# Kernel optimization log

Hardware: AMD Instinct MI355X
Metric: run time of the kernel (lower is better)

The kernel has to match this reference:

```python
import jax, jax.numpy as jnp
import numpy as np

NUM_EXPERTS = 8
TOP_K = 2
D_MODEL = 1024
D_FF = 4096
TOKENS = 8192


def setup_inputs() -> dict:
    key = jax.random.key(0)
    ks = jax.random.split(key, 7)
    s_in = 1.0 / np.sqrt(D_MODEL)
    s_ff = 1.0 / np.sqrt(D_FF)
    return {
        "x": jax.random.normal(ks[0], (TOKENS, D_MODEL), dtype=jnp.float32),
        "gate_w": jax.random.normal(ks[1], (D_MODEL, NUM_EXPERTS), dtype=jnp.float32) * s_in,
        "gate_b": jnp.zeros((NUM_EXPERTS,), dtype=jnp.float32),
        "w1": jax.random.normal(ks[2], (NUM_EXPERTS, D_MODEL, D_FF), dtype=jnp.float32) * s_in,
        "b1": jnp.zeros((NUM_EXPERTS, D_FF), dtype=jnp.float32),
        "w2": jax.random.normal(ks[3], (NUM_EXPERTS, D_FF, D_MODEL), dtype=jnp.float32) * s_ff,
        "b2": jnp.zeros((NUM_EXPERTS, D_MODEL), dtype=jnp.float32),
    }


def reference(x, gate_w, gate_b, w1, b1, w2, b2):
    # gate: softmax over experts, then top-k routing
    probs = jax.nn.softmax(x @ gate_w + gate_b, axis=-1)  # [T, E]
    topk_p, topk_i = jax.lax.top_k(probs, TOP_K)          # [T, K]
    T, E = probs.shape
    # dense per-token combine weights: zero for unrouted experts
    comb = jnp.zeros((T, E), dtype=x.dtype).at[jnp.arange(T)[:, None], topk_i].set(topk_p)
    out = jnp.zeros_like(x)
    for e in range(E):  # small fixed expert loop; math identical to masked gather/scatter
        h = jax.nn.silu(x @ w1[e] + b1[e])                # [T, D_FF]
        out = out + comb[:, e:e + 1] * (h @ w2[e] + b2[e])
    return out
```

## Files before the change

kernel.cpp:

```cpp
#include <hip/hip_runtime.h>
#include <hip/hip_bf16.h>
#include <math.h>

#define TOKENS 8192
#define DMODEL 1024
#define DFF    4096
#define NEXP   8
#define ESTRIDE   8448
#define MAX_SLOTS 72
#define BK 64

typedef __bf16 bf16;
typedef bf16  bf16x4 __attribute__((ext_vector_type(4)));
typedef bf16  bf16x8 __attribute__((ext_vector_type(8)));
typedef float f32x4  __attribute__((ext_vector_type(4)));

__device__ __forceinline__ void gload16(const bf16* g, bf16* l) {
    __builtin_amdgcn_global_load_lds(
        (const __attribute__((address_space(1))) void*)g,
        (__attribute__((address_space(3))) void*)l,
        16, 0, 0);
}

__global__ __launch_bounds__(256) void gate_kernel(
    const float* __restrict__ x, const float* __restrict__ gw, const float* __restrict__ gb,
    int2* __restrict__ topk_i, float2* __restrict__ topk_p, bf16* __restrict__ xb)
{
    int wid  = (blockIdx.x * blockDim.x + threadIdx.x) >> 6;
    int lane = threadIdx.x & 63;
    if (wid >= TOKENS) return;
    const float* xr = x + (size_t)wid * DMODEL;
    bf16* xbr = xb + (size_t)wid * DMODEL;
    float a0=0,a1=0,a2=0,a3=0,a4=0,a5=0,a6=0,a7=0;
    #pragma unroll
    for (int i = 0; i < 4; ++i) {
        int cq = i*256 + lane*4;
        float4 xv = *(const float4*)(xr + cq);
        bf16x4 xc = { (bf16)xv.x, (bf16)xv.y, (bf16)xv.z, (bf16)xv.w };
        *(bf16x4*)(xbr + cq) = xc;
        #pragma unroll
        for (int j = 0; j < 4; ++j) {
            float xe = (j==0)?xv.x:(j==1)?xv.y:(j==2)?xv.z:xv.w;
            const float4* g = (const float4*)(gw + (size_t)(cq + j) * NEXP);
            float4 g0 = g[0], g1 = g[1];
            a0 += xe * g0.x; a1 += xe * g0.y; a2 += xe * g0.z; a3 += xe * g0.w;
            a4 += xe * g1.x; a5 += xe * g1.y; a6 += xe * g1.z; a7 += xe * g1.w;
        }
    }
    #pragma unroll
    for (int off = 32; off; off >>= 1) {
        a0 += __shfl_xor(a0, off); a1 += __shfl_xor(a1, off);
        a2 += __shfl_xor(a2, off); a3 += __shfl_xor(a3, off);
        a4 += __shfl_xor(a4, off); a5 += __shfl_xor(a5, off);
        a6 += __shfl_xor(a6, off); a7 += __shfl_xor(a7, off);
    }
    if (lane == 0) {
        float l[NEXP] = { a0+gb[0], a1+gb[1], a2+gb[2], a3+gb[3],
                          a4+gb[4], a5+gb[5], a6+gb[6], a7+gb[7] };
        float m = l[0];
        #pragma unroll
        for (int e = 1; e < NEXP; ++e) m = fmaxf(m, l[e]);
        float p[NEXP], s = 0.f;
        #pragma unroll
        for (int e = 0; e < NEXP; ++e) { p[e] = expf(l[e] - m); s += p[e]; }
        float inv = 1.0f / s;
        int i1 = 0; float b1v = p[0];
        #pragma unroll
        for (int e = 1; e < NEXP; ++e) if (p[e] > b1v) { b1v = p[e]; i1 = e; }
        int i2 = -1; float b2v = -1.f;
        #pragma unroll
        for (int e = 0; e < NEXP; ++e) if (e != i1 && p[e] > b2v) { b2v = p[e]; i2 = e; }
        topk_i[wid] = make_int2(i1, i2);
        topk_p[wid] = make_float2(b1v * inv, b2v * inv);
    }
}

__global__ __launch_bounds__(64) void compact_kernel(
    const int2* __restrict__ topk_i, const float2* __restrict__ topk_p,
    int* __restrict__ counts, int* __restrict__ token_ids, float* __restrict__ pair_p)
{
    int e = blockIdx.x;
    int lane = threadIdx.x;
    int base = 0;
    for (int it = 0; it < TOKENS/64; ++it) {
        int t = it*64 + lane;
        int2 ki = topk_i[t];
        bool hit = (ki.x == e) || (ki.y == e);
        int which = (ki.y == e) ? 1 : 0;
        unsigned long long m = __ballot(hit);
        if (hit) {
            int idx = base + __popcll(m & ((1ull << lane) - 1ull));
            float2 kp = topk_p[t];
            token_ids[e*ESTRIDE + idx] = t | (which << 13);
            pair_p   [e*ESTRIDE + idx] = which ? kp.y : kp.x;
        }
        base += __popcll(m);
    }
    if (lane == 0) counts[e] = base;
}

__global__ void build_slots(const int* __restrict__ counts, int* n_slots,
                            int* slot_e, int* slot_row0, int* slot_gbase)
{
    __shared__ int sc[8], spb[9], stb[9];
    int t = threadIdx.x;
    if (t < 8) sc[t] = counts[t];
    __syncthreads();
    if (t == 0) {
        int pb = 0, tb = 0;
        for (int e = 0; e < NEXP; ++e) {
            spb[e] = pb; stb[e] = tb;
            pb += ((sc[e] + 127) >> 7) << 7;
            tb += (sc[e] + 255) >> 8;
        }
        spb[8] = pb; stb[8] = tb;
        *n_slots = tb;
    }
    __syncthreads();
    if (t < stb[8]) { int e = 0; while (t >= stb[e+1]) ++e;
        slot_e[t] = e; slot_row0[t] = (t - stb[e]) << 8; slot_gbase[t] = spb[e]; }
}

__global__ __launch_bounds__(256) void transpose_cvt(
    const float* __restrict__ src, bf16* __restrict__ dst, int R, int C)
{
    __shared__ bf16 tile[64 * 72];
    int e = blockIdx.z;
    int c0 = blockIdx.x * 64, r0 = blockIdx.y * 64;
    const float* s = src + (size_t)e * R * C;
    bf16* d = dst + (size_t)e * R * C;
    int t = threadIdx.x;
    {
        int r = t >> 2, q = t & 3;
        const float4* sp = (const float4*)(s + (size_t)(r0 + r) * C + c0 + q * 16);
        float4 v0 = sp[0], v1 = sp[1], v2 = sp[2], v3 = sp[3];
        bf16x8 p0, p1;
        p0[0]=(bf16)v0.x; p0[1]=(bf16)v0.y; p0[2]=(bf16)v0.z; p0[3]=(bf16)v0.w;
        p0[4]=(bf16)v1.x; p0[5]=(bf16)v1.y; p0[6]=(bf16)v1.z; p0[7]=(bf16)v1.w;
        p1[0]=(bf16)v2.x; p1[1]=(bf16)v2.y; p1[2]=(bf16)v2.z; p1[3]=(bf16)v2.w;
        p1[4]=(bf16)v3.x; p1[5]=(bf16)v3.y; p1[6]=(bf16)v3.z; p1[7]=(bf16)v3.w;
        bf16* w = tile + r * 72 + (q ^ (r >> 4)) * 16;
        *(bf16x8*)w = p0; *(bf16x8*)(w + 8) = p1;
    }
    __syncthreads();
    {
        int c = t >> 2, rq = t & 3;
        int gc = c >> 4, cl = c & 15;
        bf16x8 q0, q1;
        #pragma unroll
        for (int k = 0; k < 8; ++k) {
            q0[k] = tile[(rq*16 + k) * 72 + (gc ^ rq) * 16 + cl];
            q1[k] = tile[(rq*16 + 8 + k) * 72 + (gc ^ rq) * 16 + cl];
        }
        bf16* dp = d + (size_t)(c0 + c) * R + r0 + rq * 16;
        *(bf16x8*)dp = q0;
        *(bf16x8*)(dp + 8) = q1;
    }
}

__global__ __launch_bounds__(512, 2) void moe_gemm1(
    const bf16* __restrict__ Xb, const bf16* __restrict__ Bt,
    const float* __restrict__ bias, bf16* __restrict__ Hout,
    const int* __restrict__ token_ids,
    const int* __restrict__ slot_e, const int* __restrict__ slot_row0,
    const int* __restrict__ slot_gbase, const int* __restrict__ n_slots,
    const int* __restrict__ counts)
{
    constexpr int K = DMODEL, N = DFF, NJT = N / 256, NT = K / BK, NITER = NT / 2;

    int nwg = gridDim.x, bid = blockIdx.x;
    int wid = (bid & 7) * (nwg >> 3) + (bid >> 3);
    int slot = wid / NJT;
    if (slot >= *n_slots) return;
    int jt = wid % NJT;
    int e = slot_e[slot], row0 = slot_row0[slot], gbase = slot_gbase[slot];
    int cnt = counts[e];
    int pad_e = (cnt + 127) & ~127;
    int tlb = e * ESTRIDE;

    __shared__ __align__(16) bf16 shm[65536];

    int t = threadIdx.x, lane = t & 63, wv = t >> 6;
    int wm = wv >> 2, wn = wv & 3;
    int lr = lane & 15, kq = lane >> 4;
    int bh = wn >> 1, bro = (wn & 1) * 64;

    int aoff[2][2]; int boff[2][2];
    const bf16* Bbase = Bt + (size_t)e * N * K;
    int g8 = ((lane & 7) ^ (lane >> 3)) * 8;
    #pragma unroll
    for (int h = 0; h < 2; ++h)
        #pragma unroll
        for (int q = 0; q < 2; ++q) {
            int rloc = h*128 + wv*16 + q*8 + (lane >> 3);
            int tok = token_ids[tlb + row0 + rloc] & 0x1FFF;
            aoff[h][q] = tok * DMODEL + g8;
            boff[h][q] = (jt*256 + rloc) * K + g8;
        }

    f32x4 acc[8][4] = {};
    bf16x8 breg[4][2];

    #define STAGE_A(S, H, T) do { int _t = ((T) < NT ? (T) : 0) * BK;                   \
        gload16(Xb + aoff[H][0] + _t, shm + (((S)*2+(H))*128 + wv*16    ) * BK);        \
        gload16(Xb + aoff[H][1] + _t, shm + (((S)*2+(H))*128 + wv*16 + 8) * BK); } while(0)
    #define STAGE_B(S, H, T) do { int _t = ((T) < NT ? (T) : 0) * BK;                           \
        gload16(Bbase + boff[H][0] + _t, shm + 32768 + (((S)*2+(H))*128 + wv*16    ) * BK);     \
        gload16(Bbase + boff[H][1] + _t, shm + 32768 + (((S)*2+(H))*128 + wv*16 + 8) * BK); } while(0)

    STAGE_A(0,0,0); STAGE_A(0,1,0); STAGE_B(0,0,0); STAGE_B(0,1,0);
    STAGE_B(1,0,1); STAGE_B(1,1,1);
    asm volatile("s_waitcnt vmcnt(4)" ::: "memory");
    __builtin_amdgcn_s_barrier();

    #define LOAD_A(S, Q)                                                             \
        _Pragma("unroll") for (int mi = 0; mi < 2; ++mi)                             \
            _Pragma("unroll") for (int kk = 0; kk < 2; ++kk)                         \
                areg[mi][kk] = *(const bf16x8*)(shm +                                \
                    (((S)*2+wm)*128 + ((Q)*2+mi)*16 + lr) * BK +                     \
                    ((kk*4+kq) ^ (lr & 7)) * 8);
    #define MFMA_Q(Q)                                                                \
        __builtin_amdgcn_s_setprio(1);                                               \
        _Pragma("unroll") for (int mi = 0; mi < 2; ++mi)                             \
            _Pragma("unroll") for (int n = 0; n < 4; ++n)                            \
                _Pragma("unroll") for (int kk = 0; kk < 2; ++kk)                     \
                    acc[(Q)*2+mi][n] = __builtin_amdgcn_mfma_f32_16x16x32_bf16(      \
                        areg[mi][kk], breg[n][kk], acc[(Q)*2+mi][n], 0, 0, 0);       \
        __builtin_amdgcn_s_setprio(0);

    #define PHASE2(S, Q2, STAGE_CODE, DO_WAIT)                                       \
    {                                                                                \
        bf16x8 areg[2][2];                                                           \
        if ((Q2) == 0) {                                                             \
            _Pragma("unroll") for (int n = 0; n < 4; ++n)                            \
                _Pragma("unroll") for (int kk = 0; kk < 2; ++kk)                     \
                    breg[n][kk] = *(const bf16x8*)(shm + 32768 +                     \
                        (((S)*2+bh)*128 + bro + n*16 + lr) * BK +                    \
                        ((kk*4+kq) ^ (lr & 7)) * 8);                                 \
        }                                                                            \
        LOAD_A(S, (Q2)*2)                                                            \
        STAGE_CODE;                                                                  \
        asm volatile("" ::: "memory");                                               \
        __builtin_amdgcn_s_barrier();                                                \
        MFMA_Q((Q2)*2)                                                               \
        LOAD_A(S, (Q2)*2+1)                                                          \
        MFMA_Q((Q2)*2+1)                                                             \
        if (DO_WAIT) asm volatile("s_waitcnt vmcnt(4)" ::: "memory");                \
        asm volatile("" ::: "memory");                                               \
        __builtin_amdgcn_s_barrier();                                                \
    }

    for (int i = 0; i < NITER; ++i) {
        int TO = 2*i+1, TE2 = 2*i+2, TO2 = 2*i+3;
        PHASE2(0, 0, { STAGE_A(1,0,TO);  STAGE_A(1,1,TO);  }, 0)
        PHASE2(0, 1, { STAGE_B(0,0,TE2); STAGE_B(0,1,TE2); }, 1)
        PHASE2(1, 0, { STAGE_A(0,0,TE2); STAGE_A(0,1,TE2); }, 0)
        PHASE2(1, 1, { STAGE_B(1,0,TO2); STAGE_B(1,1,TO2); }, 1)
    }
    asm volatile("s_waitcnt vmcnt(0)" ::: "memory");
    #undef PHASE2
    #undef MFMA_Q
    #undef LOAD_A
    #undef STAGE_A
    #undef STAGE_B

    int lro = kq * 4;
    float bv[4];
    #pragma unroll
    for (int n = 0; n < 4; ++n)
        bv[n] = bias[e * DFF + jt*256 + wn*64 + n*16 + lr];
    #pragma unroll
    for (int m = 0; m < 8; ++m)
        #pragma unroll
        for (int reg = 0; reg < 4; ++reg) {
            int rl = wm*128 + m*16 + lro + reg;
            if (row0 + rl < pad_e) {
                size_t hrow = (size_t)(gbase + row0 + rl);
                #pragma unroll
                for (int n = 0; n < 4; ++n) {
                    int col = jt*256 + wn*64 + n*16 + lr;
                    float v = acc[m][n][reg] + bv[n];
                    v = v / (1.0f + __expf(-v));
                    __builtin_nontemporal_store((bf16)v, &Hout[hrow * DFF + col]);
                }
            }
        }
}

__global__ __launch_bounds__(512, 2) void moe_gemm2(
    const bf16* __restrict__ Ah, const bf16* __restrict__ Bt,
    const float* __restrict__ bias, bf16* __restrict__ pbuf,
    const int* __restrict__ token_ids, const float* __restrict__ pair_p,
    const int* __restrict__ slot_e, const int* __restrict__ slot_row0,
    const int* __restrict__ slot_gbase, const int* __restrict__ n_slots,
    const int* __restrict__ counts)
{
    constexpr int K = DFF, N = DMODEL, NJT = N / 128;
    constexpr int KSPL = 2, KCH = K / KSPL, NT = KCH / BK;

    int nwg = gridDim.x, bid = blockIdx.x;
    int wid = (bid & 7) * (nwg >> 3) + (bid >> 3);
    int slot = wid / (NJT * KSPL);
    if (slot >= *n_slots) return;
    int rem = wid % (NJT * KSPL);
    int jt = rem / KSPL, split = rem % KSPL;
    int kbase = split * KCH;
    int e = slot_e[slot], row0 = slot_row0[slot], gbase = slot_gbase[slot];
    int cnt = counts[e];
    int tlb = e * ESTRIDE;

    __shared__ __align__(16) bf16 shm[73728];

    int t = threadIdx.x, lane = t & 63, wv = t >> 6;
    int wm4 = wv >> 1, wn2 = wv & 1;
    int lr = lane & 15, kq = lane >> 4;
    int g8 = ((lane & 7) ^ (lane >> 3)) * 8;

    int aoff[4], boff[2];
    const bf16* Bbase = Bt + (size_t)e * N * K;
    #pragma unroll
    for (int q = 0; q < 4; ++q) {
        int rloc = wv*32 + q*8 + (lane >> 3);
        aoff[q] = (gbase + row0 + rloc) * DFF + kbase + g8;
    }
    #pragma unroll
    for (int q = 0; q < 2; ++q) {
        int rloc = wv*16 + q*8 + (lane >> 3);
        boff[q] = (jt*128 + rloc) * K + kbase + g8;
    }

    f32x4 acc[4][4] = {};

    #define ST2(S, T) do { int _t = ((T) < NT ? (T) : 0) * BK;                        \
        _Pragma("unroll") for (int q = 0; q < 4; ++q)                                 \
            gload16(Ah + aoff[q] + _t, shm + (S)*16384 + (wv*32 + q*8)*BK);           \
        _Pragma("unroll") for (int q = 0; q < 2; ++q)                                 \
            gload16(Bbase + boff[q] + _t, shm + 49152 + (S)*8192 + (wv*16 + q*8)*BK); \
        } while (0)

    ST2(0, 0); ST2(1, 1);
    int cs = 0, ps = 2;
    for (int tt = 0; tt < NT; ++tt) {
        ST2(ps, tt + 2);
        asm volatile("s_waitcnt vmcnt(12)" ::: "memory");
        __builtin_amdgcn_s_barrier();
        bf16x8 areg[4][2], breg[4][2];
        #pragma unroll
        for (int m = 0; m < 4; ++m)
            #pragma unroll
            for (int kk = 0; kk < 2; ++kk)
                areg[m][kk] = *(const bf16x8*)(shm + cs*16384 +
                    (wm4*64 + m*16 + lr)*BK + ((kk*4+kq) ^ (lr & 7))*8);
        #pragma unroll
        for (int n = 0; n < 4; ++n)
            #pragma unroll
            for (int kk = 0; kk < 2; ++kk)
                breg[n][kk] = *(const bf16x8*)(shm + 49152 + cs*8192 +
                    (wn2*64 + n*16 + lr)*BK + ((kk*4+kq) ^ (lr & 7))*8);
        __builtin_amdgcn_s_setprio(1);
        #pragma unroll
        for (int m = 0; m < 4; ++m)
            #pragma unroll
            for (int n = 0; n < 4; ++n)
                #pragma unroll
                for (int kk = 0; kk < 2; ++kk)
                    acc[m][n] = __builtin_amdgcn_mfma_f32_16x16x32_bf16(
                        areg[m][kk], breg[n][kk], acc[m][n], 0, 0, 0);
        __builtin_amdgcn_s_setprio(0);
        asm volatile("" ::: "memory");
        __builtin_amdgcn_s_barrier();
        cs = (cs == 2) ? 0 : cs + 1;
        ps = (ps == 2) ? 0 : ps + 1;
    }
    asm volatile("s_waitcnt vmcnt(0)" ::: "memory");
    #undef ST2

    float bv[4];
    #pragma unroll
    for (int n = 0; n < 4; ++n)
        bv[n] = (split == 0) ? bias[e * DMODEL + jt*128 + wn2*64 + n*16 + lr] : 0.0f;
    #pragma unroll
    for (int m = 0; m < 4; ++m)
        #pragma unroll
        for (int reg = 0; reg < 4; ++reg) {
            int rl = wm4*64 + m*16 + kq*4 + reg;
            if (row0 + rl < cnt) {
                int pr = tlb + row0 + rl;
                int tw = token_ids[pr];
                int tok = tw & 0x1FFF, wh = (tw >> 13) & 1;
                float p = pair_p[pr];
                bf16* dst = pbuf + ((size_t)(tok*4 + wh*2 + split)) * DMODEL;
                #pragma unroll
                for (int n = 0; n < 4; ++n) {
                    int col = jt*128 + wn2*64 + n*16 + lr;
                    __builtin_nontemporal_store((bf16)(p * (acc[m][n][reg] + bv[n])), &dst[col]);
                }
            }
        }
}

__global__ __launch_bounds__(256) void combine_kernel(
    const bf16* __restrict__ pbuf, float* __restrict__ out)
{
    int wid  = (blockIdx.x * 256 + threadIdx.x) >> 6;
    int lane = threadIdx.x & 63;
    const bf16* pr = pbuf + (size_t)wid * 4 * DMODEL;
    float* o = out + (size_t)wid * DMODEL;
    #pragma unroll
    for (int i = 0; i < 2; ++i) {
        int c = (i*64 + lane) * 8;
        bf16x8 v0 = *(const bf16x8*)(pr + c);
        bf16x8 v1 = *(const bf16x8*)(pr + DMODEL + c);
        bf16x8 v2 = *(const bf16x8*)(pr + 2*DMODEL + c);
        bf16x8 v3 = *(const bf16x8*)(pr + 3*DMODEL + c);
        f32x4 r0, r1;
        #pragma unroll
        for (int k = 0; k < 4; ++k)
            r0[k] = (float)v0[k] + (float)v1[k] + (float)v2[k] + (float)v3[k];
        #pragma unroll
        for (int k = 0; k < 4; ++k)
            r1[k] = (float)v0[4+k] + (float)v1[4+k] + (float)v2[4+k] + (float)v3[4+k];
        *(f32x4*)(o + c) = r0;
        *(f32x4*)(o + c + 4) = r1;
    }
}

extern "C" void kernel_launch(void* const* d_in, const int* in_sizes, int n_in,
                              void* d_out, int out_size, void* d_ws, size_t ws_size,
                              hipStream_t stream)
{
    const float* x  = (const float*)d_in[0];
    const float* gw = (const float*)d_in[1];
    const float* gb = (const float*)d_in[2];
    const float* w1 = (const float*)d_in[3];
    const float* b1 = (const float*)d_in[4];
    const float* w2 = (const float*)d_in[5];
    const float* b2 = (const float*)d_in[6];
    float* out = (float*)d_out;

    const size_t W1T_OFF = 0;
    const size_t W2T_OFF = 67108864;
    const size_t H_OFF   = 134217728;
    const size_t S_OFF   = H_OFF + (size_t)17408 * DFF * 2;
    const size_t WS_NEEDED = S_OFF + 4096 + 2*(NEXP*ESTRIDE*4) + 2*(TOKENS*8);
    if (ws_size < WS_NEEDED) return;

    char* ws = (char*)d_ws;
    bf16*  w1t  = (bf16*)(ws + W1T_OFF);
    bf16*  pbuf = (bf16*)(ws + W1T_OFF);
    bf16*  w2t  = (bf16*)(ws + W2T_OFF);
    bf16*  xb   = (bf16*)(ws + W2T_OFF);
    bf16*  h    = (bf16*)(ws + H_OFF);
    char*  S    = ws + S_OFF;
    int*   counts    = (int*)(S + 0);
    int*   n_slots   = (int*)(S + 64);
    int*   slot_e    = (int*)(S + 128);
    int*   slot_row0 = (int*)(S + 512);
    int*   slot_gbase= (int*)(S + 896);
    int*   token_ids = (int*)(S + 4096);
    float* pair_p    = (float*)(S + 4096 + NEXP*ESTRIDE*4);
    int2*  topk_i    = (int2*)(S + 4096 + 2*(NEXP*ESTRIDE*4));
    float2* topk_p   = (float2*)(S + 4096 + 2*(NEXP*ESTRIDE*4) + TOKENS*8);

    transpose_cvt<<<dim3(DFF/64, DMODEL/64, NEXP), dim3(256), 0, stream>>>(w1, w1t, DMODEL, DFF);

    gate_kernel<<<TOKENS * 64 / 256, 256, 0, stream>>>(x, gw, gb, topk_i, topk_p, xb);
    compact_kernel<<<NEXP, 64, 0, stream>>>(topk_i, topk_p, counts, token_ids, pair_p);
    build_slots<<<1, 128, 0, stream>>>(counts, n_slots, slot_e, slot_row0, slot_gbase);

    moe_gemm1<<<MAX_SLOTS * (DFF/256), 512, 0, stream>>>(
        xb, w1t, b1, h, token_ids, slot_e, slot_row0, slot_gbase, n_slots, counts);

    transpose_cvt<<<dim3(DMODEL/64, DFF/64, NEXP), dim3(256), 0, stream>>>(w2, w2t, DFF, DMODEL);

    moe_gemm2<<<MAX_SLOTS * (DMODEL/128) * 2, 512, 0, stream>>>(
        h, w2t, b2, pbuf, token_ids, pair_p, slot_e, slot_row0, slot_gbase, n_slots, counts);

    combine_kernel<<<TOKENS * 64 / 256, 256, 0, stream>>>(pbuf, out);
}
```

Before: 577.6 us.

## Widen moe_gemm2 tile to 256x256 with double buffering and staged A loads

Doubles the N tile of the second expert GEMM from 128 to 256 columns, so each workgroup computes a 256x256 output block with 8x4 accumulators per wave in a 2x4 wave layout. Shared memory switches from triple to double buffering to stay within LDS. A fragments are loaded in four stages interleaved with MFMA bursts. The wider tile raises arithmetic intensity and halves the grid, at the cost of more accumulator registers, possible spills under launch_bounds(512,2), and less latency hiding from the shallower pipeline.

```diff
diff --git a/kernel.cpp b/kernel.cpp
--- a/kernel.cpp
+++ b/kernel.cpp
@@ -295,7 +295,7 @@
     const int* __restrict__ slot_gbase, const int* __restrict__ n_slots,
     const int* __restrict__ counts)
 {
-    constexpr int K = DFF, N = DMODEL, NJT = N / 128;
+    constexpr int K = DFF, N = DMODEL, NJT = N / 256;
     constexpr int KSPL = 2, KCH = K / KSPL, NT = KCH / BK;
 
     int nwg = gridDim.x, bid = blockIdx.x;
@@ -309,68 +309,65 @@
     int cnt = counts[e];
     int tlb = e * ESTRIDE;
 
-    __shared__ __align__(16) bf16 shm[73728];
+    __shared__ __align__(16) bf16 shm[65536];
 
     int t = threadIdx.x, lane = t & 63, wv = t >> 6;
-    int wm4 = wv >> 1, wn2 = wv & 1;
+    int wm = wv >> 2, wn = wv & 3;
     int lr = lane & 15, kq = lane >> 4;
     int g8 = ((lane & 7) ^ (lane >> 3)) * 8;
 
-    int aoff[4], boff[2];
+    int aoff[4], boff[4];
     const bf16* Bbase = Bt + (size_t)e * N * K;
     #pragma unroll
     for (int q = 0; q < 4; ++q) {
         int rloc = wv*32 + q*8 + (lane >> 3);
         aoff[q] = (gbase + row0 + rloc) * DFF + kbase + g8;
-    }
-    #pragma unroll
-    for (int q = 0; q < 2; ++q) {
-        int rloc = wv*16 + q*8 + (lane >> 3);
-        boff[q] = (jt*128 + rloc) * K + kbase + g8;
-    }
-
-    f32x4 acc[4][4] = {};
+        boff[q] = (jt*256 + rloc) * K + kbase + g8;
+    }
+
+    f32x4 acc[8][4] = {};
 
     #define ST2(S, T) do { int _t = ((T) < NT ? (T) : 0) * BK;                        \
-        _Pragma("unroll") for (int q = 0; q < 4; ++q)                                 \
+        _Pragma("unroll") for (int q = 0; q < 4; ++q) {                               \
             gload16(Ah + aoff[q] + _t, shm + (S)*16384 + (wv*32 + q*8)*BK);           \
-        _Pragma("unroll") for (int q = 0; q < 2; ++q)                                 \
-            gload16(Bbase + boff[q] + _t, shm + 49152 + (S)*8192 + (wv*16 + q*8)*BK); \
+            gload16(Bbase + boff[q] + _t, shm + 32768 + (S)*16384 + (wv*32+q*8)*BK); }\
         } while (0)
 
-    ST2(0, 0); ST2(1, 1);
-    int cs = 0, ps = 2;
+    ST2(0, 0);
     for (int tt = 0; tt < NT; ++tt) {
-        ST2(ps, tt + 2);
-        asm volatile("s_waitcnt vmcnt(12)" ::: "memory");
+        int cs = tt & 1;
+        ST2(cs ^ 1, tt + 1);
+        asm volatile("s_waitcnt vmcnt(8)" ::: "memory");
         __builtin_amdgcn_s_barrier();
-        bf16x8 areg[4][2], breg[4][2];
-        #pragma unroll
-        for (int m = 0; m < 4; ++m)
-            #pragma unroll
-            for (int kk = 0; kk < 2; ++kk)
-                areg[m][kk] = *(const bf16x8*)(shm + cs*16384 +
-                    (wm4*64 + m*16 + lr)*BK + ((kk*4+kq) ^ (lr & 7))*8);
+        bf16x8 breg[4][2];
         #pragma unroll
         for (int n = 0; n < 4; ++n)
             #pragma unroll
             for (int kk = 0; kk < 2; ++kk)
-                breg[n][kk] = *(const bf16x8*)(shm + 49152 + cs*8192 +
-                    (wn2*64 + n*16 + lr)*BK + ((kk*4+kq) ^ (lr & 7))*8);
-        __builtin_amdgcn_s_setprio(1);
-        #pragma unroll
-        for (int m = 0; m < 4; ++m)
+                breg[n][kk] = *(const bf16x8*)(shm + 32768 + cs*16384 +
+                    (wn*64 + n*16 + lr)*BK + ((kk*4+kq) ^ (lr & 7))*8);
+        #pragma unroll
+        for (int Q = 0; Q < 4; ++Q) {
+            bf16x8 areg[2][2];
             #pragma unroll
-            for (int n = 0; n < 4; ++n)
+            for (int mi = 0; mi < 2; ++mi)
                 #pragma unroll
                 for (int kk = 0; kk < 2; ++kk)
-                    acc[m][n] = __builtin_amdgcn_mfma_f32_16x16x32_bf16(
-                        areg[m][kk], breg[n][kk], acc[m][n], 0, 0, 0);
-        __builtin_amdgcn_s_setprio(0);
+                    areg[mi][kk] = *(const bf16x8*)(shm + cs*16384 +
+                        (wm*128 + (Q*2+mi)*16 + lr)*BK + ((kk*4+kq) ^ (lr & 7))*8);
+            __builtin_amdgcn_s_setprio(1);
+            #pragma unroll
+            for (int mi = 0; mi < 2; ++mi)
+                #pragma unroll
+                for (int n = 0; n < 4; ++n)
+                    #pragma unroll
+                    for (int kk = 0; kk < 2; ++kk)
+                        acc[Q*2+mi][n] = __builtin_amdgcn_mfma_f32_16x16x32_bf16(
+                            areg[mi][kk], breg[n][kk], acc[Q*2+mi][n], 0, 0, 0);
+            __builtin_amdgcn_s_setprio(0);
+        }
         asm volatile("" ::: "memory");
         __builtin_amdgcn_s_barrier();
-        cs = (cs == 2) ? 0 : cs + 1;
-        ps = (ps == 2) ? 0 : ps + 1;
     }
     asm volatile("s_waitcnt vmcnt(0)" ::: "memory");
     #undef ST2
@@ -378,12 +375,12 @@
     float bv[4];
     #pragma unroll
     for (int n = 0; n < 4; ++n)
-        bv[n] = (split == 0) ? bias[e * DMODEL + jt*128 + wn2*64 + n*16 + lr] : 0.0f;
-    #pragma unroll
-    for (int m = 0; m < 4; ++m)
+        bv[n] = (split == 0) ? bias[e * DMODEL + jt*256 + wn*64 + n*16 + lr] : 0.0f;
+    #pragma unroll
+    for (int m = 0; m < 8; ++m)
         #pragma unroll
         for (int reg = 0; reg < 4; ++reg) {
-            int rl = wm4*64 + m*16 + kq*4 + reg;
+            int rl = wm*128 + m*16 + kq*4 + reg;
             if (row0 + rl < cnt) {
                 int pr = tlb + row0 + rl;
                 int tw = token_ids[pr];
@@ -392,7 +389,7 @@
                 bf16* dst = pbuf + ((size_t)(tok*4 + wh*2 + split)) * DMODEL;
                 #pragma unroll
                 for (int n = 0; n < 4; ++n) {
-                    int col = jt*128 + wn2*64 + n*16 + lr;
+                    int col = jt*256 + wn*64 + n*16 + lr;
                     __builtin_nontemporal_store((bf16)(p * (acc[m][n][reg] + bv[n])), &dst[col]);
                 }
             }
@@ -473,7 +470,7 @@
 
     transpose_cvt<<<dim3(DMODEL/64, DFF/64, NEXP), dim3(256), 0, stream>>>(w2, w2t, DFF, DMODEL);
 
-    moe_gemm2<<<MAX_SLOTS * (DMODEL/128) * 2, 512, 0, stream>>>(
+    moe_gemm2<<<MAX_SLOTS * (DMODEL/256) * 2, 512, 0, stream>>>(
         h, w2t, b2, pbuf, token_ids, pair_p, slot_e, slot_row0, slot_gbase, n_slots, counts);
 
     combine_kernel<<<TOKENS * 64 / 256, 256, 0, stream>>>(pbuf, out);
```

After: 594.6 us. 1.03x slower.
